# Optimization experiments

Measured on AMD Instinct MI355X. Metric: run time of the kernel, lower is better.

Reference implementation:

```python
import jax, jax.numpy as jnp
import numpy as np

N_NODES = 50000
N_EDGES = 800000
IN_DIM, HID_DIM, OUT_DIM = 128, 128, 64


def _sage_conv(x, src, dst, W_l, W_r, b, num_nodes):
    # mean aggregation of source-node features onto destination nodes
    msg = x[src]  # [E, d] gather
    summed = jax.ops.segment_sum(msg, dst, num_segments=num_nodes)  # [N, d]
    deg = jax.ops.segment_sum(jnp.ones((src.shape[0],), dtype=x.dtype), dst,
                              num_segments=num_nodes)  # [N]
    agg = summed / jnp.maximum(deg, 1.0)[:, None]
    # SAGEConv: lin_l(agg) + lin_r(x); bias only on lin_l (PyG default)
    return agg @ W_l + b + x @ W_r


def setup_inputs() -> dict:
    key = jax.random.key(0)
    k = jax.random.split(key, 8)
    def glorot(kk, shape):
        lim = float(np.sqrt(6.0 / (shape[0] + shape[1])))
        return jax.random.uniform(kk, shape, jnp.float32, -lim, lim)
    return {
        "x": jax.random.normal(k[0], (N_NODES, IN_DIM), jnp.float32),
        "edge_index": jax.random.randint(k[1], (2, N_EDGES), 0, N_NODES, jnp.int64),
        "W1_l": glorot(k[2], (IN_DIM, HID_DIM)),
        "W1_r": glorot(k[3], (IN_DIM, HID_DIM)),
        "b1": jnp.zeros((HID_DIM,), jnp.float32),
        "W2_l": glorot(k[4], (HID_DIM, OUT_DIM)),
        "W2_r": glorot(k[5], (HID_DIM, OUT_DIM)),
        "b2": jnp.zeros((OUT_DIM,), jnp.float32),
    }


def reference(x, edge_index, W1_l, W1_r, b1, W2_l, W2_r, b2):
    src, dst = edge_index[0], edge_index[1]
    n = x.shape[0]
    h = _sage_conv(x, src, dst, W1_l, W1_r, b1, n)
    h = jax.nn.relu(h)
    # dropout is identity in eval mode
    out = _sage_conv(h, src, dst, W2_l, W2_r, b2, n)
    return out
```

## Files before the change

kernel.cpp:

```cpp
#include <hip/hip_runtime.h>
#include <hip/hip_bf16.h>


#define BLK 256

typedef __attribute__((ext_vector_type(8))) short short8;
typedef __attribute__((ext_vector_type(4))) float f32x4;

__device__ inline unsigned short f2bf(float f) {
    unsigned int u = __builtin_bit_cast(unsigned int, f);
    u += 0x7fffu + ((u >> 16) & 1u);
    return (unsigned short)(u >> 16);
}
__device__ inline float bf2f(unsigned short h) {
    return __builtin_bit_cast(float, ((unsigned int)h) << 16);
}


__global__ __launch_bounds__(BLK) void deg_count_kernel(const int* __restrict__ dst,
                                                        int E, int* __restrict__ deg) {
    int e = blockIdx.x * BLK + threadIdx.x;
    if (e < E) atomicAdd(&deg[dst[e]], 1);
}

__global__ __launch_bounds__(BLK) void partial_sum_kernel(const int* __restrict__ deg,
                                                          int n, int* __restrict__ partials) {
    __shared__ int s[BLK];
    int t = threadIdx.x;
    int idx = blockIdx.x * BLK + t;
    s[t] = (idx < n) ? deg[idx] : 0;
    __syncthreads();
    for (int o = BLK / 2; o > 0; o >>= 1) {
        if (t < o) s[t] += s[t + o];
        __syncthreads();
    }
    if (t == 0) partials[blockIdx.x] = s[0];
}

__global__ __launch_bounds__(BLK) void scan_partials_kernel(int* __restrict__ partials, int n) {
    __shared__ int s[BLK];
    int t = threadIdx.x;
    int v = (t < n) ? partials[t] : 0;
    s[t] = v;
    __syncthreads();
    int sum = v;
    for (int o = 1; o < BLK; o <<= 1) {
        int other = (t >= o) ? s[t - o] : 0;
        __syncthreads();
        sum += other;
        s[t] = sum;
        __syncthreads();
    }
    if (t < n) partials[t] = sum - v;
}

__global__ __launch_bounds__(BLK) void chunk_scan_kernel(const int* __restrict__ deg,
                                                         const int* __restrict__ partials,
                                                         int n, int* __restrict__ row_start) {
    __shared__ int s[BLK];
    int t = threadIdx.x;
    int idx = blockIdx.x * BLK + t;
    int v = (idx < n) ? deg[idx] : 0;
    s[t] = v;
    __syncthreads();
    int sum = v;
    for (int o = 1; o < BLK; o <<= 1) {
        int other = (t >= o) ? s[t - o] : 0;
        __syncthreads();
        sum += other;
        s[t] = sum;
        __syncthreads();
    }
    if (idx < n) row_start[idx] = (sum - v) + partials[blockIdx.x];
}

__global__ __launch_bounds__(BLK) void fill_kernel(const int* __restrict__ src,
                                                   const int* __restrict__ dst, int E,
                                                   const int* __restrict__ row_start,
                                                   int* __restrict__ cursor,
                                                   int* __restrict__ csr_src) {
    int e = blockIdx.x * BLK + threadIdx.x;
    if (e >= E) return;
    int d = dst[e];
    int pos = atomicAdd(&cursor[d], 1);
    csr_src[row_start[d] + pos] = src[e];
}


__global__ __launch_bounds__(BLK) void f32_to_bf16_kernel(const float* __restrict__ in,
                                                          unsigned short* __restrict__ out,
                                                          int nquad) {
    int i = blockIdx.x * BLK + threadIdx.x;
    if (i >= nquad) return;
    float4 v = ((const float4*)in)[i];
    ushort4 o;
    o.x = f2bf(v.x); o.y = f2bf(v.y); o.z = f2bf(v.z); o.w = f2bf(v.w);
    ((ushort4*)out)[i] = o;
}

__global__ __launch_bounds__(BLK) void pack_w_kernel(const float* __restrict__ W,
                                                     unsigned short* __restrict__ P,
                                                     int K, int Ncol) {
    int t = blockIdx.x * BLK + threadIdx.x;
    if (t >= K * Ncol) return;
    int j = t & 7;
    int lane = (t >> 3) & 63;
    int rest = t >> 9;
    int nt = Ncol >> 4;
    int n16 = rest % nt, kb = rest / nt;
    int k = kb * 32 + (lane >> 4) * 8 + j;
    int c = n16 * 16 + (lane & 15);
    P[t] = f2bf(W[(size_t)k * Ncol + c]);
}


__global__ __launch_bounds__(BLK) void agg_bf16_kernel(const unsigned short* __restrict__ feat,
                                                       const int* __restrict__ row_start,
                                                       const int* __restrict__ deg,
                                                       const int* __restrict__ csr_src,
                                                       unsigned short* __restrict__ out,
                                                       int n_nodes) {
    int gid = blockIdx.x * (BLK / 64) + (threadIdx.x >> 6);
    int lane = threadIdx.x & 63;
    if (gid >= n_nodes) return;
    int start = row_start[gid];
    int cnt = deg[gid];
    const unsigned int* fp = (const unsigned int*)feat;
    float a0 = 0.f, a1 = 0.f, b0 = 0.f, b1 = 0.f;
    float c0 = 0.f, c1 = 0.f, d0 = 0.f, d1 = 0.f;
    int e = 0;
    for (; e + 4 <= cnt; e += 4) {
        int s0 = csr_src[start + e];
        int s1 = csr_src[start + e + 1];
        int s2 = csr_src[start + e + 2];
        int s3 = csr_src[start + e + 3];
        unsigned int v0 = fp[(size_t)s0 * 64 + lane];
        unsigned int v1 = fp[(size_t)s1 * 64 + lane];
        unsigned int v2 = fp[(size_t)s2 * 64 + lane];
        unsigned int v3 = fp[(size_t)s3 * 64 + lane];
        a0 += bf2f((unsigned short)v0); a1 += bf2f((unsigned short)(v0 >> 16));
        b0 += bf2f((unsigned short)v1); b1 += bf2f((unsigned short)(v1 >> 16));
        c0 += bf2f((unsigned short)v2); c1 += bf2f((unsigned short)(v2 >> 16));
        d0 += bf2f((unsigned short)v3); d1 += bf2f((unsigned short)(v3 >> 16));
    }
    for (; e < cnt; ++e) {
        int s0 = csr_src[start + e];
        unsigned int v0 = fp[(size_t)s0 * 64 + lane];
        a0 += bf2f((unsigned short)v0); a1 += bf2f((unsigned short)(v0 >> 16));
    }
    float inv = 1.0f / fmaxf((float)cnt, 1.0f);
    float rx = (a0 + b0 + c0 + d0) * inv;
    float ry = (a1 + b1 + c1 + d1) * inv;
    unsigned int packed = (unsigned int)f2bf(rx) | ((unsigned int)f2bf(ry) << 16);
    ((unsigned int*)out)[(size_t)gid * 64 + lane] = packed;
}


template <int NCOL, bool RELU, bool OUT_BF16>
__global__ __launch_bounds__(BLK) void gemm_mfma_kernel(const unsigned short* __restrict__ A1,
                                                        const unsigned short* __restrict__ A2,
                                                        const unsigned short* __restrict__ Pl,
                                                        const unsigned short* __restrict__ Pr,
                                                        const float* __restrict__ bias,
                                                        void* __restrict__ outp, int M) {
    constexpr int NT = NCOL / 16;
    const int wave = threadIdx.x >> 6, lane = threadIdx.x & 63;
    const int r0 = blockIdx.x * 128 + wave * 32;
    const int arow = lane & 15, kgrp = lane >> 4;

    f32x4 acc[2][NT];
#pragma unroll
    for (int h = 0; h < 2; h++)
#pragma unroll
        for (int n = 0; n < NT; n++) acc[h][n] = (f32x4){0.f, 0.f, 0.f, 0.f};

    const int ra = min(r0 + arow, M - 1);
    const int rb = min(r0 + 16 + arow, M - 1);

#pragma unroll
    for (int mat = 0; mat < 2; ++mat) {
        const unsigned short* A = mat ? A2 : A1;
        const unsigned short* P = mat ? Pr : Pl;
        const unsigned short* Aa = A + (size_t)ra * 128 + kgrp * 8;
        const unsigned short* Ab = A + (size_t)rb * 128 + kgrp * 8;
#pragma unroll
        for (int kb = 0; kb < 4; ++kb) {
            short8 afa = *(const short8*)(Aa + kb * 32);
            short8 afb = *(const short8*)(Ab + kb * 32);
            const unsigned short* Pk = P + (size_t)kb * NT * 512 + lane * 8;
#pragma unroll
            for (int n = 0; n < NT; ++n) {
                short8 wf = *(const short8*)(Pk + n * 512);
                acc[0][n] = __builtin_amdgcn_mfma_f32_16x16x32_bf16(afa, wf, acc[0][n], 0, 0, 0);
                acc[1][n] = __builtin_amdgcn_mfma_f32_16x16x32_bf16(afb, wf, acc[1][n], 0, 0, 0);
            }
        }
    }

#pragma unroll
    for (int n = 0; n < NT; ++n) {
        int col = n * 16 + arow;
        float bv = bias[col];
#pragma unroll
        for (int h = 0; h < 2; ++h) {
#pragma unroll
            for (int i = 0; i < 4; ++i) {
                int row = r0 + h * 16 + kgrp * 4 + i;
                if (row < M) {
                    float v = acc[h][n][i] + bv;
                    if (RELU) v = fmaxf(v, 0.f);
                    if (OUT_BF16)
                        ((unsigned short*)outp)[(size_t)row * NCOL + col] = f2bf(v);
                    else
                        ((float*)outp)[(size_t)row * NCOL + col] = v;
                }
            }
        }
    }
}


extern "C" void kernel_launch(void* const* d_in, const int* in_sizes, int n_in,
                              void* d_out, int out_size, void* d_ws, size_t ws_size,
                              hipStream_t stream) {
    const float* x   = (const float*)d_in[0];
    const int*   ei  = (const int*)d_in[1];
    const float* W1l = (const float*)d_in[2];
    const float* W1r = (const float*)d_in[3];
    const float* b1  = (const float*)d_in[4];
    const float* W2l = (const float*)d_in[5];
    const float* W2r = (const float*)d_in[6];
    const float* b2  = (const float*)d_in[7];
    float* out = (float*)d_out;

    const int N = in_sizes[0] / 128;
    const int E = in_sizes[1] / 2;
    const int* src = ei;
    const int* dst = ei + E;

    char* ws = (char*)d_ws;
    size_t off = 0;
    auto carve = [&](size_t bytes) {
        void* p = ws + off;
        off += (bytes + 255) & ~(size_t)255;
        return p;
    };
    int* deg       = (int*)carve((size_t)N * 4);
    int* cursor    = (int*)carve((size_t)N * 4);
    int* row_start = (int*)carve((size_t)N * 4);
    int* partials  = (int*)carve(256 * 4);
    int* csr_src   = (int*)carve((size_t)E * 4);
    unsigned short* xb   = (unsigned short*)carve((size_t)N * 128 * 2);
    unsigned short* aggb = (unsigned short*)carve((size_t)N * 128 * 2);
    unsigned short* hb   = (unsigned short*)carve((size_t)N * 128 * 2);
    unsigned short* P1l  = (unsigned short*)carve(128 * 128 * 2);
    unsigned short* P1r  = (unsigned short*)carve(128 * 128 * 2);
    unsigned short* P2l  = (unsigned short*)carve(128 * 64 * 2);
    unsigned short* P2r  = (unsigned short*)carve(128 * 64 * 2);

    hipMemsetAsync(deg, 0, (size_t)N * 4, stream);
    hipMemsetAsync(cursor, 0, (size_t)N * 4, stream);

    const int nquad = N * 128 / 4;
    f32_to_bf16_kernel<<<(nquad + BLK - 1) / BLK, BLK, 0, stream>>>(x, xb, nquad);
    pack_w_kernel<<<(128 * 128 + BLK - 1) / BLK, BLK, 0, stream>>>(W1l, P1l, 128, 128);
    pack_w_kernel<<<(128 * 128 + BLK - 1) / BLK, BLK, 0, stream>>>(W1r, P1r, 128, 128);
    pack_w_kernel<<<(128 * 64 + BLK - 1) / BLK, BLK, 0, stream>>>(W2l, P2l, 128, 64);
    pack_w_kernel<<<(128 * 64 + BLK - 1) / BLK, BLK, 0, stream>>>(W2r, P2r, 128, 64);

    const int nchunk = (N + BLK - 1) / BLK;
    deg_count_kernel<<<(E + BLK - 1) / BLK, BLK, 0, stream>>>(dst, E, deg);
    partial_sum_kernel<<<nchunk, BLK, 0, stream>>>(deg, N, partials);
    scan_partials_kernel<<<1, BLK, 0, stream>>>(partials, nchunk);
    chunk_scan_kernel<<<nchunk, BLK, 0, stream>>>(deg, partials, N, row_start);
    fill_kernel<<<(E + BLK - 1) / BLK, BLK, 0, stream>>>(src, dst, E, row_start, cursor, csr_src);

    const int aggGrid = (N + 3) / 4;
    const int gemmGrid = (N + 127) / 128;

    agg_bf16_kernel<<<aggGrid, BLK, 0, stream>>>(xb, row_start, deg, csr_src, aggb, N);
    gemm_mfma_kernel<128, true, true><<<gemmGrid, BLK, 0, stream>>>(aggb, xb, P1l, P1r, b1, hb, N);
    agg_bf16_kernel<<<aggGrid, BLK, 0, stream>>>(hb, row_start, deg, csr_src, aggb, N);
    gemm_mfma_kernel<64, false, false><<<gemmGrid, BLK, 0, stream>>>(aggb, hb, P2l, P2r, b2, out, N);
}
```

Before: 298.6 us.

## Batch weight packing, merge memsets, and use shuffle-broadcast indices in aggregation

The four weight-packing launches become one kernel, and the two memsets become one by placing the degree and cursor buffers next to each other. The aggregation kernel now loads up to 64 neighbour indices per wave with one coalesced load and broadcasts them with shuffles. It also unrolls 8 feature gathers per step with 8 independent accumulators to raise memory-level parallelism. The CSR fill store becomes an atomicExch, which adds atomic overhead to a store that already had a unique address.

After: 303.8 us. No clear change (+1.8%).

```diff
diff --git a/kernel.cpp b/kernel.cpp
--- a/kernel.cpp
+++ b/kernel.cpp
@@ -83,7 +83,7 @@
     if (e >= E) return;
     int d = dst[e];
     int pos = atomicAdd(&cursor[d], 1);
-    csr_src[row_start[d] + pos] = src[e];
+    atomicExch(&csr_src[row_start[d] + pos], src[e]);
 }
 
 
@@ -98,19 +98,31 @@
     ((ushort4*)out)[i] = o;
 }
 
-__global__ __launch_bounds__(BLK) void pack_w_kernel(const float* __restrict__ W,
-                                                     unsigned short* __restrict__ P,
-                                                     int K, int Ncol) {
+__global__ __launch_bounds__(BLK) void pack_all_w_kernel(const float* __restrict__ W1l,
+                                                         const float* __restrict__ W1r,
+                                                         const float* __restrict__ W2l,
+                                                         const float* __restrict__ W2r,
+                                                         unsigned short* __restrict__ P1l,
+                                                         unsigned short* __restrict__ P1r,
+                                                         unsigned short* __restrict__ P2l,
+                                                         unsigned short* __restrict__ P2r) {
     int t = blockIdx.x * BLK + threadIdx.x;
-    if (t >= K * Ncol) return;
-    int j = t & 7;
-    int lane = (t >> 3) & 63;
-    int rest = t >> 9;
+    const float* W;
+    unsigned short* P;
+    int Ncol, local;
+    if (t < 16384)      { W = W1l; P = P1l; Ncol = 128; local = t; }
+    else if (t < 32768) { W = W1r; P = P1r; Ncol = 128; local = t - 16384; }
+    else if (t < 40960) { W = W2l; P = P2l; Ncol = 64;  local = t - 32768; }
+    else if (t < 49152) { W = W2r; P = P2r; Ncol = 64;  local = t - 40960; }
+    else return;
+    int j = local & 7;
+    int lane = (local >> 3) & 63;
+    int rest = local >> 9;
     int nt = Ncol >> 4;
     int n16 = rest % nt, kb = rest / nt;
     int k = kb * 32 + (lane >> 4) * 8 + j;
     int c = n16 * 16 + (lane & 15);
-    P[t] = f2bf(W[(size_t)k * Ncol + c]);
+    P[local] = f2bf(W[(size_t)k * Ncol + c]);
 }
 
 
@@ -126,32 +138,39 @@
     int start = row_start[gid];
     int cnt = deg[gid];
     const unsigned int* fp = (const unsigned int*)feat;
-    float a0 = 0.f, a1 = 0.f, b0 = 0.f, b1 = 0.f;
-    float c0 = 0.f, c1 = 0.f, d0 = 0.f, d1 = 0.f;
-    int e = 0;
-    for (; e + 4 <= cnt; e += 4) {
-        int s0 = csr_src[start + e];
-        int s1 = csr_src[start + e + 1];
-        int s2 = csr_src[start + e + 2];
-        int s3 = csr_src[start + e + 3];
-        unsigned int v0 = fp[(size_t)s0 * 64 + lane];
-        unsigned int v1 = fp[(size_t)s1 * 64 + lane];
-        unsigned int v2 = fp[(size_t)s2 * 64 + lane];
-        unsigned int v3 = fp[(size_t)s3 * 64 + lane];
-        a0 += bf2f((unsigned short)v0); a1 += bf2f((unsigned short)(v0 >> 16));
-        b0 += bf2f((unsigned short)v1); b1 += bf2f((unsigned short)(v1 >> 16));
-        c0 += bf2f((unsigned short)v2); c1 += bf2f((unsigned short)(v2 >> 16));
-        d0 += bf2f((unsigned short)v3); d1 += bf2f((unsigned short)(v3 >> 16));
-    }
-    for (; e < cnt; ++e) {
-        int s0 = csr_src[start + e];
-        unsigned int v0 = fp[(size_t)s0 * 64 + lane];
-        a0 += bf2f((unsigned short)v0); a1 += bf2f((unsigned short)(v0 >> 16));
-    }
+    float ax[8], ay[8];
+#pragma unroll
+    for (int j = 0; j < 8; j++) { ax[j] = 0.f; ay[j] = 0.f; }
+
+    for (int base = 0; base < cnt; base += 64) {
+        int rem = cnt - base;
+        int m = rem < 64 ? rem : 64;
+        int idx = csr_src[start + base + (lane < m ? lane : m - 1)];
+        int e = 0;
+        for (; e + 8 <= m; e += 8) {
+            unsigned int v[8];
+#pragma unroll
+            for (int j = 0; j < 8; j++) {
+                int s = __shfl(idx, e + j);
+                v[j] = fp[(size_t)s * 64 + lane];
+            }
+#pragma unroll
+            for (int j = 0; j < 8; j++) {
+                ax[j] += bf2f((unsigned short)v[j]);
+                ay[j] += bf2f((unsigned short)(v[j] >> 16));
+            }
+        }
+        for (; e < m; ++e) {
+            int s = __shfl(idx, e);
+            unsigned int v = fp[(size_t)s * 64 + lane];
+            ax[0] += bf2f((unsigned short)v);
+            ay[0] += bf2f((unsigned short)(v >> 16));
+        }
+    }
+    float sx = ((ax[0] + ax[1]) + (ax[2] + ax[3])) + ((ax[4] + ax[5]) + (ax[6] + ax[7]));
+    float sy = ((ay[0] + ay[1]) + (ay[2] + ay[3])) + ((ay[4] + ay[5]) + (ay[6] + ay[7]));
     float inv = 1.0f / fmaxf((float)cnt, 1.0f);
-    float rx = (a0 + b0 + c0 + d0) * inv;
-    float ry = (a1 + b1 + c1 + d1) * inv;
-    unsigned int packed = (unsigned int)f2bf(rx) | ((unsigned int)f2bf(ry) << 16);
+    unsigned int packed = (unsigned int)f2bf(sx * inv) | ((unsigned int)f2bf(sy * inv) << 16);
     ((unsigned int*)out)[(size_t)gid * 64 + lane] = packed;
 }
 
@@ -245,8 +264,8 @@
         off += (bytes + 255) & ~(size_t)255;
         return p;
     };
-    int* deg       = (int*)carve((size_t)N * 4);
-    int* cursor    = (int*)carve((size_t)N * 4);
+    int* deg       = (int*)carve((size_t)2 * N * 4);
+    int* cursor    = deg + N;
     int* row_start = (int*)carve((size_t)N * 4);
     int* partials  = (int*)carve(256 * 4);
     int* csr_src   = (int*)carve((size_t)E * 4);
@@ -258,15 +277,11 @@
     unsigned short* P2l  = (unsigned short*)carve(128 * 64 * 2);
     unsigned short* P2r  = (unsigned short*)carve(128 * 64 * 2);
 
-    hipMemsetAsync(deg, 0, (size_t)N * 4, stream);
-    hipMemsetAsync(cursor, 0, (size_t)N * 4, stream);
+    hipMemsetAsync(deg, 0, (size_t)2 * N * 4, stream);
 
     const int nquad = N * 128 / 4;
     f32_to_bf16_kernel<<<(nquad + BLK - 1) / BLK, BLK, 0, stream>>>(x, xb, nquad);
-    pack_w_kernel<<<(128 * 128 + BLK - 1) / BLK, BLK, 0, stream>>>(W1l, P1l, 128, 128);
-    pack_w_kernel<<<(128 * 128 + BLK - 1) / BLK, BLK, 0, stream>>>(W1r, P1r, 128, 128);
-    pack_w_kernel<<<(128 * 64 + BLK - 1) / BLK, BLK, 0, stream>>>(W2l, P2l, 128, 64);
-    pack_w_kernel<<<(128 * 64 + BLK - 1) / BLK, BLK, 0, stream>>>(W2r, P2r, 128, 64);
+    pack_all_w_kernel<<<192, BLK, 0, stream>>>(W1l, W1r, W2l, W2r, P1l, P1r, P2l, P2r);
 
     const int nchunk = (N + BLK - 1) / BLK;
     deg_count_kernel<<<(E + BLK - 1) / BLK, BLK, 0, stream>>>(dst, E, deg);
```
